# Kernel optimization log

Hardware: AMD Instinct MI355X
Metric: run time of the kernel (lower is better)

The kernel has to match this reference:

```python
import jax, jax.numpy as jnp
import numpy as np

NUM_HEADS, HEAD_SIZE = 8, 80
C = NUM_HEADS * HEAD_SIZE  # 640
GROUPS = 32
EPS = 1e-5


def group_norm(x, gamma, beta):
    b, h, w, c = x.shape
    xg = x.reshape(b, h, w, GROUPS, c // GROUPS)
    mean = xg.mean(axis=(1, 2, 4), keepdims=True)
    var = xg.var(axis=(1, 2, 4), keepdims=True)
    xg = (xg - mean) * jax.lax.rsqrt(var + EPS)
    return xg.reshape(b, h, w, c) * gamma + beta


def layer_norm(x, gamma, beta):
    mean = x.mean(axis=-1, keepdims=True)
    var = x.var(axis=-1, keepdims=True)
    return (x - mean) * jax.lax.rsqrt(var + EPS) * gamma + beta


def cross_attention(x, ctx, wq, wk, wv, wo, bo):
    # x: [B,S,C], ctx: [B,T,Cc]
    b, s, _ = x.shape
    t = ctx.shape[1]
    q = (x @ wq).reshape(b, s, NUM_HEADS, HEAD_SIZE)
    k = (ctx @ wk).reshape(b, t, NUM_HEADS, HEAD_SIZE)
    v = (ctx @ wv).reshape(b, t, NUM_HEADS, HEAD_SIZE)
    scale = HEAD_SIZE ** -0.5
    score = jnp.einsum('bqnh,bknh->bnqk', q, k) * scale
    weights = jax.nn.softmax(score, axis=-1)
    attn = jnp.einsum('bnqk,bknh->bqnh', weights, v)
    return attn.reshape(b, s, C) @ wo + bo


def geglu(x, w, b):
    p = x @ w + b
    xh, gate = p[..., :2560], p[..., 2560:]
    tanh_res = jnp.tanh(gate * 0.7978845608 * (1.0 + 0.044715 * gate * gate))
    return xh * 0.5 * gate * (1.0 + tanh_res)


def setup_inputs() -> dict:
    key = jax.random.key(0)
    ks = iter(jax.random.split(key, 32))
    rn = lambda shape, s=0.02: jax.random.normal(next(ks), shape, dtype=jnp.float32) * s
    inp = {
        'x': jax.random.normal(next(ks), (8, 32, 32, 640), dtype=jnp.float32),
        'context': jax.random.normal(next(ks), (8, 77, 768), dtype=jnp.float32),
        'gn_gamma': jnp.ones((640,), jnp.float32), 'gn_beta': jnp.zeros((640,), jnp.float32),
        'proj_in_w': rn((640, 640)), 'proj_in_b': jnp.zeros((640,), jnp.float32),
        'ln1_g': jnp.ones((640,), jnp.float32), 'ln1_b': jnp.zeros((640,), jnp.float32),
        'a1_q': rn((640, 640)), 'a1_k': rn((640, 640)), 'a1_v': rn((640, 640)),
        'a1_o': rn((640, 640)), 'a1_ob': jnp.zeros((640,), jnp.float32),
        'ln2_g': jnp.ones((640,), jnp.float32), 'ln2_b': jnp.zeros((640,), jnp.float32),
        'a2_q': rn((640, 640)), 'a2_k': rn((768, 640)), 'a2_v': rn((768, 640)),
        'a2_o': rn((640, 640)), 'a2_ob': jnp.zeros((640,), jnp.float32),
        'ln3_g': jnp.ones((640,), jnp.float32), 'ln3_b': jnp.zeros((640,), jnp.float32),
        'ff1_w': rn((640, 5120)), 'ff1_b': jnp.zeros((5120,), jnp.float32),
        'ff2_w': rn((2560, 640)), 'ff2_b': jnp.zeros((640,), jnp.float32),
        'proj_out_w': rn((640, 640)), 'proj_out_b': jnp.zeros((640,), jnp.float32),
    }
    return inp


def reference(x, context, gn_gamma, gn_beta, proj_in_w, proj_in_b,
              ln1_g, ln1_b, a1_q, a1_k, a1_v, a1_o, a1_ob,
              ln2_g, ln2_b, a2_q, a2_k, a2_v, a2_o, a2_ob,
              ln3_g, ln3_b, ff1_w, ff1_b, ff2_w, ff2_b,
              proj_out_w, proj_out_b):
    b, h, w, c = x.shape
    # GroupNorm + 1x1 conv proj_in (== dense over channels)
    y = group_norm(x, gn_gamma, gn_beta)
    y = y @ proj_in_w + proj_in_b
    y = y.reshape(b, h * w, c)
    # Transformer block
    t = cross_attention(layer_norm(y, ln1_g, ln1_b), layer_norm(y, ln1_g, ln1_b), a1_q, a1_k, a1_v, a1_o, a1_ob) + y
    t = cross_attention(layer_norm(t, ln2_g, ln2_b), context, a2_q, a2_k, a2_v, a2_o, a2_ob) + t
    t = geglu(layer_norm(t, ln3_g, ln3_b), ff1_w, ff1_b) @ ff2_w + ff2_b + t
    # proj_out (1x1 conv) + residual
    t = t.reshape(b, h, w, c)
    return t @ proj_out_w + proj_out_b + x
```

## Files before the change

kernel.cpp:

```cpp
#include <hip/hip_runtime.h>
#include <hip/hip_bf16.h>
#include <math.h>

typedef unsigned short u16;
typedef unsigned int u32;
typedef __attribute__((ext_vector_type(8))) short bf16x8;
typedef __attribute__((ext_vector_type(4))) float f32x4;

__device__ __forceinline__ u16 f2b(float f) {
    union { float f; unsigned u; } v; v.f = f;
    unsigned r = v.u + 0x7fffu + ((v.u >> 16) & 1u);
    return (u16)(r >> 16);
}
__device__ __forceinline__ float b2f(u16 h) {
    union { unsigned u; float f; } v; v.u = ((unsigned)h) << 16; return v.f;
}

__device__ __forceinline__ void gld16(const u16* gp, u16* lp) {
    auto g = (const __attribute__((address_space(1))) u32*)gp;
    auto l = (__attribute__((address_space(3))) u32*)lp;
    __builtin_amdgcn_global_load_lds(g, l, 16, 0, 0);
}

__device__ __forceinline__ int swz(int row, int q) { return (q + (row >> 1)) & 3; }

struct GemmP {
    const u16* A; const float* Af; const u16* B;
    const float* bias; const float* res;
    float* Cf; u16* Cb;
    int M, N, K, lda, ldb, ldc;
    float alpha;
};

__global__ __launch_bounds__(256) void gemm_bt(GemmP p) {
    __shared__ u16 As[128 * 32];
    __shared__ u16 Bs[128 * 32];
    const int tid = threadIdx.x;
    const int m0 = blockIdx.y * 128, n0 = blockIdx.x * 128;
    const int lane = tid & 63, wave = tid >> 6;
    const int quad = lane >> 4, l16 = lane & 15;
    const int wr = (wave >> 1) * 64, wc = (wave & 1) * 64;
    const int srow = lane >> 2, pcb = lane & 3;

    f32x4 acc[4][4];
#pragma unroll
    for (int i = 0; i < 4; i++)
#pragma unroll
        for (int j = 0; j < 4; j++) acc[i][j] = (f32x4){0.f, 0.f, 0.f, 0.f};

    for (int k0 = 0; k0 < p.K; k0 += 32) {
        if (p.Af) {
            int row = tid >> 1, half = tid & 1;
            const float* src = p.Af + (long)(m0 + row) * p.lda + k0 + half * 16;
            u16 tmp[16];
#pragma unroll
            for (int i2 = 0; i2 < 4; i2++) {
                float4 f = *(const float4*)(src + i2 * 4);
                tmp[i2 * 4 + 0] = f2b(f.x); tmp[i2 * 4 + 1] = f2b(f.y);
                tmp[i2 * 4 + 2] = f2b(f.z); tmp[i2 * 4 + 3] = f2b(f.w);
            }
            *(uint4*)&As[row * 32 + swz(row, 2 * half) * 8]     = *(uint4*)tmp;
            *(uint4*)&As[row * 32 + swz(row, 2 * half + 1) * 8] = *(uint4*)(tmp + 8);
#pragma unroll
            for (int j = 0; j < 2; j++) {
                int rbase = wave * 32 + j * 16;
                int r = rbase + srow;
                int lcb = (pcb - (r >> 1)) & 3;
                gld16(p.B + (long)(n0 + r) * p.ldb + k0 + lcb * 8, &Bs[rbase * 32]);
            }
        } else {
#pragma unroll
            for (int j = 0; j < 2; j++) {
                int rbase = wave * 32 + j * 16;
                int r = rbase + srow;
                int lcb = (pcb - (r >> 1)) & 3;
                gld16(p.A + (long)(m0 + r) * p.lda + k0 + lcb * 8, &As[rbase * 32]);
                gld16(p.B + (long)(n0 + r) * p.ldb + k0 + lcb * 8, &Bs[rbase * 32]);
            }
        }
        __syncthreads();

        bf16x8 af[4], bfr[4];
#pragma unroll
        for (int mi = 0; mi < 4; mi++) {
            int row = wr + mi * 16 + l16;
            af[mi] = *(const bf16x8*)&As[row * 32 + swz(row, quad) * 8];
        }
#pragma unroll
        for (int ni = 0; ni < 4; ni++) {
            int row = wc + ni * 16 + l16;
            bfr[ni] = *(const bf16x8*)&Bs[row * 32 + swz(row, quad) * 8];
        }
#pragma unroll
        for (int mi = 0; mi < 4; mi++)
#pragma unroll
            for (int ni = 0; ni < 4; ni++)
                acc[mi][ni] = __builtin_amdgcn_mfma_f32_16x16x32_bf16(af[mi], bfr[ni], acc[mi][ni], 0, 0, 0);
        __syncthreads();
    }

#pragma unroll
    for (int mi = 0; mi < 4; mi++) {
#pragma unroll
        for (int ni = 0; ni < 4; ni++) {
#pragma unroll
            for (int r = 0; r < 4; r++) {
                int row = m0 + wr + mi * 16 + quad * 4 + r;
                int col = n0 + wc + ni * 16 + l16;
                if (row < p.M && col < p.N) {
                    float v = acc[mi][ni][r] * p.alpha;
                    if (p.bias) v += p.bias[col];
                    long idx = (long)row * p.ldc + col;
                    if (p.res) v += p.res[idx];
                    if (p.Cf) p.Cf[idx] = v; else p.Cb[idx] = f2b(v);
                }
            }
        }
    }
}

struct GegluP {
    const u16* A; const u16* Bx; const u16* Bg;
    const float* bx; const float* bg;
    u16* H;
    int K, lda, ldb, ldh;
};

__global__ __launch_bounds__(256) void gemm_geglu(GegluP p) {
    __shared__ u16 As[128 * 32];
    __shared__ u16 Bxs[128 * 32];
    __shared__ u16 Bgs[128 * 32];
    const int tid = threadIdx.x;
    const int m0 = blockIdx.y * 128, n0 = blockIdx.x * 128;
    const int lane = tid & 63, wave = tid >> 6;
    const int quad = lane >> 4, l16 = lane & 15;
    const int wr = (wave >> 1) * 64, wc = (wave & 1) * 64;
    const int srow = lane >> 2, pcb = lane & 3;

    f32x4 ax[4][4], ag[4][4];
#pragma unroll
    for (int i = 0; i < 4; i++)
#pragma unroll
        for (int j = 0; j < 4; j++) { ax[i][j] = (f32x4){0.f,0.f,0.f,0.f}; ag[i][j] = (f32x4){0.f,0.f,0.f,0.f}; }

    for (int k0 = 0; k0 < p.K; k0 += 32) {
#pragma unroll
        for (int j = 0; j < 2; j++) {
            int rbase = wave * 32 + j * 16;
            int r = rbase + srow;
            int lcb = (pcb - (r >> 1)) & 3;
            gld16(p.A  + (long)(m0 + r) * p.lda + k0 + lcb * 8, &As[rbase * 32]);
            gld16(p.Bx + (long)(n0 + r) * p.ldb + k0 + lcb * 8, &Bxs[rbase * 32]);
            gld16(p.Bg + (long)(n0 + r) * p.ldb + k0 + lcb * 8, &Bgs[rbase * 32]);
        }
        __syncthreads();

        bf16x8 af[4], bxf[4], bgf[4];
#pragma unroll
        for (int mi = 0; mi < 4; mi++) {
            int row = wr + mi * 16 + l16;
            af[mi] = *(const bf16x8*)&As[row * 32 + swz(row, quad) * 8];
        }
#pragma unroll
        for (int ni = 0; ni < 4; ni++) {
            int row = wc + ni * 16 + l16;
            bxf[ni] = *(const bf16x8*)&Bxs[row * 32 + swz(row, quad) * 8];
            bgf[ni] = *(const bf16x8*)&Bgs[row * 32 + swz(row, quad) * 8];
        }
#pragma unroll
        for (int mi = 0; mi < 4; mi++)
#pragma unroll
            for (int ni = 0; ni < 4; ni++) {
                ax[mi][ni] = __builtin_amdgcn_mfma_f32_16x16x32_bf16(af[mi], bxf[ni], ax[mi][ni], 0, 0, 0);
                ag[mi][ni] = __builtin_amdgcn_mfma_f32_16x16x32_bf16(af[mi], bgf[ni], ag[mi][ni], 0, 0, 0);
            }
        __syncthreads();
    }

#pragma unroll
    for (int mi = 0; mi < 4; mi++) {
#pragma unroll
        for (int ni = 0; ni < 4; ni++) {
#pragma unroll
            for (int r = 0; r < 4; r++) {
                int row = m0 + wr + mi * 16 + quad * 4 + r;
                int col = wc + ni * 16 + l16;
                float xh = ax[mi][ni][r] + p.bx[n0 + col];
                float g  = ag[mi][ni][r] + p.bg[n0 + col];
                float u  = 0.7978845608f * g * (1.0f + 0.044715f * g * g);
                float s  = 1.0f / (1.0f + __expf(-2.0f * u));
                p.H[(long)row * p.ldh + n0 + col] = f2b(xh * g * s);
            }
        }
    }
}

struct FlashP {
    const u16* Q; const u16* K; const u16* V;
    u16* O;
    int ldq, ldk, ldv, ldo;
    int S, TS, nIter;
    long qBatch, kBatch;
    float scale;
};

__global__ __launch_bounds__(256, 2) void flash_attn(FlashP p) {
    __shared__ u16 shU[128 * 136];
    __shared__ u16 shV[80 * 136];
    const int z = blockIdx.z, b = z >> 3, h = z & 7;
    const int q0 = blockIdx.x * 128;
    const int tid = threadIdx.x, lane = tid & 63, w = tid >> 6;
    const int quad = lane >> 4, l16 = lane & 15;

    const u16* Qp = p.Q + (long)b * p.qBatch + (long)q0 * p.ldq + h * 80;
    const u16* Kp = p.K + (long)b * p.kBatch + h * 80;
    const u16* Vp = p.V + (long)b * p.kBatch + h * 80;

    for (int idx = tid; idx < 128 * 12; idx += 256) {
        int row = idx / 12, g = idx - row * 12;
        uint4 v = {0, 0, 0, 0};
        if (g < 10) v = *(const uint4*)(Qp + (long)row * p.ldq + g * 8);
        *(uint4*)&shU[row * 104 + g * 8] = v;
    }
    __syncthreads();
    bf16x8 qf[2][3];
#pragma unroll
    for (int mi = 0; mi < 2; mi++)
#pragma unroll
        for (int kk = 0; kk < 3; kk++)
            qf[mi][kk] = *(const bf16x8*)&shU[(w * 32 + mi * 16 + l16) * 104 + kk * 32 + quad * 8];
    __syncthreads();

    float m_[2][4], l_[2][4];
    f32x4 acc_o[2][5];
#pragma unroll
    for (int mi = 0; mi < 2; mi++) {
#pragma unroll
        for (int r = 0; r < 4; r++) { m_[mi][r] = -1e30f; l_[mi][r] = 0.f; }
#pragma unroll
        for (int ni = 0; ni < 5; ni++) acc_o[mi][ni] = (f32x4){0.f, 0.f, 0.f, 0.f};
    }

    for (int it = 0; it < p.nIter; it++) {
        const int s0 = it * 128;
        for (int idx = tid; idx < 128 * 12; idx += 256) {
            int row = idx / 12, g = idx - row * 12;
            uint4 v = {0, 0, 0, 0};
            if (g < 10 && (s0 + row) < p.TS)
                v = *(const uint4*)(Kp + (long)(s0 + row) * p.ldk + g * 8);
            *(uint4*)&shU[row * 104 + g * 8] = v;
        }
        for (int idx = tid; idx < 128 * 10; idx += 256) {
            int row = idx / 10, g = idx - row * 10;
            uint4 v = {0, 0, 0, 0};
            if ((s0 + row) < p.TS)
                v = *(const uint4*)(Vp + (long)(s0 + row) * p.ldv + g * 8);
            u16 tmp[8]; *(uint4*)tmp = v;
#pragma unroll
            for (int j = 0; j < 8; j++) shV[(g * 8 + j) * 136 + row] = tmp[j];
        }
        __syncthreads();

        f32x4 acc_s[2][8];
#pragma unroll
        for (int mi = 0; mi < 2; mi++)
#pragma unroll
            for (int ni = 0; ni < 8; ni++) acc_s[mi][ni] = (f32x4){0.f, 0.f, 0.f, 0.f};
#pragma unroll
        for (int kk = 0; kk < 3; kk++) {
            bf16x8 kf[8];
#pragma unroll
            for (int ni = 0; ni < 8; ni++)
                kf[ni] = *(const bf16x8*)&shU[(ni * 16 + l16) * 104 + kk * 32 + quad * 8];
#pragma unroll
            for (int mi = 0; mi < 2; mi++)
#pragma unroll
                for (int ni = 0; ni < 8; ni++)
                    acc_s[mi][ni] = __builtin_amdgcn_mfma_f32_16x16x32_bf16(qf[mi][kk], kf[ni], acc_s[mi][ni], 0, 0, 0);
        }
        __syncthreads();

#pragma unroll
        for (int mi = 0; mi < 2; mi++) {
#pragma unroll
            for (int ni = 0; ni < 8; ni++) {
                bool valid = (s0 + ni * 16 + l16) < p.TS;
#pragma unroll
                for (int r = 0; r < 4; r++)
                    acc_s[mi][ni][r] = valid ? acc_s[mi][ni][r] * p.scale : -1e30f;
            }
#pragma unroll
            for (int r = 0; r < 4; r++) {
                float rm = acc_s[mi][0][r];
#pragma unroll
                for (int ni = 1; ni < 8; ni++) rm = fmaxf(rm, acc_s[mi][ni][r]);
#pragma unroll
                for (int msk = 1; msk < 16; msk <<= 1) rm = fmaxf(rm, __shfl_xor(rm, msk));
                float mn = fmaxf(m_[mi][r], rm);
                float al = __expf(m_[mi][r] - mn);
                m_[mi][r] = mn;
                float rs = 0.f;
                int prow = (w * 32 + mi * 16 + quad * 4 + r) * 136;
#pragma unroll
                for (int ni = 0; ni < 8; ni++) {
                    float pv = __expf(acc_s[mi][ni][r] - mn);
                    rs += pv;
                    shU[prow + ni * 16 + l16] = f2b(pv);
                }
#pragma unroll
                for (int msk = 1; msk < 16; msk <<= 1) rs += __shfl_xor(rs, msk);
                l_[mi][r] = l_[mi][r] * al + rs;
#pragma unroll
                for (int ni = 0; ni < 5; ni++) acc_o[mi][ni][r] *= al;
            }
        }
        __syncthreads();

#pragma unroll
        for (int kk = 0; kk < 4; kk++) {
            bf16x8 vf[5], pf[2];
#pragma unroll
            for (int ni = 0; ni < 5; ni++)
                vf[ni] = *(const bf16x8*)&shV[(ni * 16 + l16) * 136 + kk * 32 + quad * 8];
#pragma unroll
            for (int mi = 0; mi < 2; mi++)
                pf[mi] = *(const bf16x8*)&shU[(w * 32 + mi * 16 + l16) * 136 + kk * 32 + quad * 8];
#pragma unroll
            for (int mi = 0; mi < 2; mi++)
#pragma unroll
                for (int ni = 0; ni < 5; ni++)
                    acc_o[mi][ni] = __builtin_amdgcn_mfma_f32_16x16x32_bf16(pf[mi], vf[ni], acc_o[mi][ni], 0, 0, 0);
        }
        __syncthreads();
    }

    u16* Op = p.O + ((long)b * p.S + q0) * p.ldo + h * 80;
#pragma unroll
    for (int mi = 0; mi < 2; mi++) {
#pragma unroll
        for (int r = 0; r < 4; r++) {
            float inv = 1.0f / l_[mi][r];
            int row = w * 32 + mi * 16 + quad * 4 + r;
#pragma unroll
            for (int ni = 0; ni < 5; ni++)
                Op[(long)row * p.ldo + ni * 16 + l16] = f2b(acc_o[mi][ni][r] * inv);
        }
    }
}

struct WT8 { const float* W[8]; u16* Wt[8]; };

__global__ void wtrans8(WT8 p, int K, int N) {
    __shared__ float tile[32][33];
    const float* W = p.W[blockIdx.z];
    u16* Wt = p.Wt[blockIdx.z];
    int n0 = blockIdx.x * 32, k0 = blockIdx.y * 32;
    int tx = threadIdx.x, ty = threadIdx.y;
#pragma unroll
    for (int i = 0; i < 4; i++) {
        int k = k0 + ty + i * 8, n = n0 + tx;
        if (k < K && n < N) tile[ty + i * 8][tx] = W[(long)k * N + n];
    }
    __syncthreads();
#pragma unroll
    for (int i = 0; i < 4; i++) {
        int n = n0 + ty + i * 8, k = k0 + tx;
        if (n < N && k < K) Wt[(long)n * K + k] = f2b(tile[tx][ty + i * 8]);
    }
}

__global__ void gn_stats(const float* __restrict__ x, float* __restrict__ stats) {
    int bid = blockIdx.x;
    int b = bid >> 5, g = bid & 31;
    const float* base = x + (long)b * 32 * 32 * 640 + g * 20;
    float s = 0.f, sq = 0.f;
    for (int idx = threadIdx.x; idx < 32 * 32 * 20; idx += 256) {
        int hw = idx / 20, c = idx - hw * 20;
        float v = base[(long)hw * 640 + c];
        s += v; sq += v * v;
    }
    __shared__ float rs[256], rq[256];
    rs[threadIdx.x] = s; rq[threadIdx.x] = sq; __syncthreads();
    for (int t = 128; t > 0; t >>= 1) {
        if (threadIdx.x < t) { rs[threadIdx.x] += rs[threadIdx.x + t]; rq[threadIdx.x] += rq[threadIdx.x + t]; }
        __syncthreads();
    }
    if (threadIdx.x == 0) {
        float mean = rs[0] / 20480.0f;
        float var = rq[0] / 20480.0f - mean * mean;
        stats[bid * 2] = mean;
        stats[bid * 2 + 1] = rsqrtf(var + 1e-5f);
    }
}

__global__ void gn_apply(const float* __restrict__ x, const float* __restrict__ stats,
                         const float* __restrict__ gamma, const float* __restrict__ beta,
                         u16* __restrict__ out) {
    long i = (long)blockIdx.x * 256 + threadIdx.x;
    int c = (int)(i % 640);
    int b = (int)(i / (32 * 32 * 640));
    int g = c / 20;
    float mean = stats[(b * 32 + g) * 2], inv = stats[(b * 32 + g) * 2 + 1];
    out[i] = f2b((x[i] - mean) * inv * gamma[c] + beta[c]);
}

__global__ void layernorm_rows(const float* __restrict__ X, const float* __restrict__ g,
                               const float* __restrict__ be, u16* __restrict__ out, int nrows) {
    int row = blockIdx.x * 4 + (threadIdx.x >> 6);
    int lane = threadIdx.x & 63;
    if (row >= nrows) return;
    const float* x = X + (long)row * 640;
    float v[10];
    float s = 0.f;
#pragma unroll
    for (int i = 0; i < 10; i++) { v[i] = x[lane + i * 64]; s += v[i]; }
#pragma unroll
    for (int m = 1; m < 64; m <<= 1) s += __shfl_xor(s, m);
    float mean = s * (1.0f / 640.0f);
    float sq = 0.f;
#pragma unroll
    for (int i = 0; i < 10; i++) { float d = v[i] - mean; sq += d * d; }
#pragma unroll
    for (int m = 1; m < 64; m <<= 1) sq += __shfl_xor(sq, m);
    float inv = rsqrtf(sq * (1.0f / 640.0f) + 1e-5f);
    u16* o = out + (long)row * 640;
#pragma unroll
    for (int i = 0; i < 10; i++) {
        int c = lane + i * 64;
        o[c] = f2b((v[i] - mean) * inv * g[c] + be[c]);
    }
}

__global__ void f2b_k(const float* __restrict__ src, u16* __restrict__ dst, long n) {
    long i = (long)blockIdx.x * 256 + threadIdx.x;
    if (i < n) dst[i] = f2b(src[i]);
}

extern "C" void kernel_launch(void* const* d_in, const int* in_sizes, int n_in,
                              void* d_out, int out_size, void* d_ws, size_t ws_size,
                              hipStream_t stream) {
    const float* x        = (const float*)d_in[0];
    const float* context  = (const float*)d_in[1];
    const float* gn_gamma = (const float*)d_in[2];
    const float* gn_beta  = (const float*)d_in[3];
    const float* proj_in_w = (const float*)d_in[4];
    const float* proj_in_b = (const float*)d_in[5];
    const float* ln1_g = (const float*)d_in[6];
    const float* ln1_b = (const float*)d_in[7];
    const float* a1_q = (const float*)d_in[8];
    const float* a1_k = (const float*)d_in[9];
    const float* a1_v = (const float*)d_in[10];
    const float* a1_o = (const float*)d_in[11];
    const float* a1_ob = (const float*)d_in[12];
    const float* ln2_g = (const float*)d_in[13];
    const float* ln2_b = (const float*)d_in[14];
    const float* a2_q = (const float*)d_in[15];
    const float* a2_k = (const float*)d_in[16];
    const float* a2_v = (const float*)d_in[17];
    const float* a2_o = (const float*)d_in[18];
    const float* a2_ob = (const float*)d_in[19];
    const float* ln3_g = (const float*)d_in[20];
    const float* ln3_b = (const float*)d_in[21];
    const float* ff1_w = (const float*)d_in[22];
    const float* ff1_b = (const float*)d_in[23];
    const float* ff2_w = (const float*)d_in[24];
    const float* ff2_b = (const float*)d_in[25];
    const float* proj_out_w = (const float*)d_in[26];
    const float* proj_out_b = (const float*)d_in[27];
    float* out = (float*)d_out;

    char* ws = (char*)d_ws;
    size_t off = 0;
    auto alloc = [&](size_t bytes) -> void* {
        void* p = ws + off;
        off += (bytes + 255) & ~(size_t)255;
        return p;
    };
    u16* Wt_pi  = (u16*)alloc(640 * 640 * 2);
    u16* Wt_qkv = (u16*)alloc((size_t)1920 * 640 * 2);
    u16* Wt_1o  = (u16*)alloc(640 * 640 * 2);
    u16* Wt_2q  = (u16*)alloc(640 * 640 * 2);
    u16* Wt_kv2 = (u16*)alloc((size_t)1280 * 768 * 2);
    u16* Wt_2o  = (u16*)alloc(640 * 640 * 2);
    u16* Wt_f1  = (u16*)alloc((size_t)5120 * 640 * 2);
    u16* Wt_f2  = (u16*)alloc((size_t)640 * 2560 * 2);
    u16* Wt_po  = (u16*)alloc(640 * 640 * 2);
    float* t    = (float*)alloc((size_t)8192 * 640 * 4);
    u16* bufA   = (u16*)alloc((size_t)8192 * 640 * 2);
    u16* big    = (u16*)alloc((size_t)8192 * 2560 * 2);
    u16* kv2b   = (u16*)alloc((size_t)616 * 1280 * 2);
    u16* ctxb   = (u16*)alloc((size_t)616 * 768 * 2);
    float* stats = (float*)alloc(256 * 2 * 4);
    (void)alloc(65536);
    u16* qkvb = big;
    u16* hb   = big;

    const float SCALE = 0.11180339887498949f;

    auto gemm1 = [&](const u16* A, const float* Af, const u16* Bt, const float* bias,
                     const float* res, float* Cf, u16* Cb, int M, int N, int K,
                     int lda, int ldb, int ldc, float alpha) {
        GemmP p{};
        p.A = A; p.Af = Af; p.B = Bt; p.bias = bias; p.res = res; p.Cf = Cf; p.Cb = Cb;
        p.M = M; p.N = N; p.K = K; p.lda = lda; p.ldb = ldb; p.ldc = ldc;
        p.alpha = alpha;
        dim3 grid((N + 127) / 128, (M + 127) / 128, 1);
        gemm_bt<<<grid, 256, 0, stream>>>(p);
    };

    {
        dim3 blk(32, 8);
        WT8 sq{};
        sq.W[0] = proj_in_w; sq.Wt[0] = Wt_pi;
        sq.W[1] = a1_q;      sq.Wt[1] = Wt_qkv;
        sq.W[2] = a1_k;      sq.Wt[2] = Wt_qkv + 640 * 640;
        sq.W[3] = a1_v;      sq.Wt[3] = Wt_qkv + 2 * 640 * 640;
        sq.W[4] = a1_o;      sq.Wt[4] = Wt_1o;
        sq.W[5] = a2_q;      sq.Wt[5] = Wt_2q;
        sq.W[6] = a2_o;      sq.Wt[6] = Wt_2o;
        sq.W[7] = proj_out_w; sq.Wt[7] = Wt_po;
        wtrans8<<<dim3(20, 20, 8), blk, 0, stream>>>(sq, 640, 640);
        WT8 kv{};
        kv.W[0] = a2_k; kv.Wt[0] = Wt_kv2;
        kv.W[1] = a2_v; kv.Wt[1] = Wt_kv2 + (size_t)640 * 768;
        wtrans8<<<dim3(20, 24, 2), blk, 0, stream>>>(kv, 768, 640);
        WT8 f1{}; f1.W[0] = ff1_w; f1.Wt[0] = Wt_f1;
        wtrans8<<<dim3(160, 20, 1), blk, 0, stream>>>(f1, 640, 5120);
        WT8 f2{}; f2.W[0] = ff2_w; f2.Wt[0] = Wt_f2;
        wtrans8<<<dim3(20, 80, 1), blk, 0, stream>>>(f2, 2560, 640);
    }

    gn_stats<<<256, 256, 0, stream>>>(x, stats);
    gn_apply<<<20480, 256, 0, stream>>>(x, stats, gn_gamma, gn_beta, bufA);
    gemm1(bufA, nullptr, Wt_pi, proj_in_b, nullptr, t, nullptr, 8192, 640, 640, 640, 640, 640, 1.0f);

    layernorm_rows<<<2048, 256, 0, stream>>>(t, ln1_g, ln1_b, bufA, 8192);
    gemm1(bufA, nullptr, Wt_qkv, nullptr, nullptr, nullptr, qkvb, 8192, 1920, 640, 640, 640, 1920, 1.0f);
    {
        FlashP p{};
        p.Q = qkvb; p.K = qkvb + 640; p.V = qkvb + 1280; p.O = bufA;
        p.ldq = 1920; p.ldk = 1920; p.ldv = 1920; p.ldo = 640;
        p.S = 1024; p.TS = 1024; p.nIter = 8;
        p.qBatch = (long)1024 * 1920; p.kBatch = (long)1024 * 1920;
        p.scale = SCALE;
        flash_attn<<<dim3(8, 1, 64), 256, 0, stream>>>(p);
    }
    gemm1(bufA, nullptr, Wt_1o, a1_ob, t, t, nullptr, 8192, 640, 640, 640, 640, 640, 1.0f);

    layernorm_rows<<<2048, 256, 0, stream>>>(t, ln2_g, ln2_b, bufA, 8192);
    f2b_k<<<1848, 256, 0, stream>>>(context, ctxb, 473088);
    gemm1(bufA, nullptr, Wt_2q, nullptr, nullptr, nullptr, qkvb, 8192, 640, 640, 640, 640, 640, 1.0f);
    gemm1(ctxb, nullptr, Wt_kv2, nullptr, nullptr, nullptr, kv2b, 616, 1280, 768, 768, 768, 1280, 1.0f);
    {
        FlashP p{};
        p.Q = qkvb; p.K = kv2b; p.V = kv2b + 640; p.O = bufA;
        p.ldq = 640; p.ldk = 1280; p.ldv = 1280; p.ldo = 640;
        p.S = 1024; p.TS = 77; p.nIter = 1;
        p.qBatch = (long)1024 * 640; p.kBatch = (long)77 * 1280;
        p.scale = SCALE;
        flash_attn<<<dim3(8, 1, 64), 256, 0, stream>>>(p);
    }
    gemm1(bufA, nullptr, Wt_2o, a2_ob, t, t, nullptr, 8192, 640, 640, 640, 640, 640, 1.0f);

    layernorm_rows<<<2048, 256, 0, stream>>>(t, ln3_g, ln3_b, bufA, 8192);
    {
        GegluP p{};
        p.A = bufA; p.Bx = Wt_f1; p.Bg = Wt_f1 + (size_t)2560 * 640;
        p.bx = ff1_b; p.bg = ff1_b + 2560;
        p.H = hb;
        p.K = 640; p.lda = 640; p.ldb = 640; p.ldh = 2560;
        gemm_geglu<<<dim3(20, 64), 256, 0, stream>>>(p);
    }
    gemm1(hb, nullptr, Wt_f2, ff2_b, t, t, nullptr, 8192, 640, 2560, 2560, 2560, 640, 1.0f);

    gemm1(nullptr, t, Wt_po, proj_out_b, x, out, nullptr, 8192, 640, 640, 640, 640, 640, 1.0f);
}
```

Before: 852.0 us.

## Double GEMM K-tile to 64, add 64-row M tile, reorder flash grid

The GEMM and GEGLU kernels now stage a 64-wide K slice per iteration with an 8-way swizzle, halving the number of barrier pairs per K loop. gemm_bt is templated on M tile size, and the N=640 GEMMs use 64-row tiles to launch more blocks and fill more CUs. The flash attention grid swaps its x and z dimensions so consecutive blocks cover different batch-heads. In exchange, LDS use per block roughly doubles, which may lower occupancy, and the smaller tiles reduce operand reuse.

```diff
diff --git a/kernel.cpp b/kernel.cpp
--- a/kernel.cpp
+++ b/kernel.cpp
@@ -22,7 +22,7 @@
     __builtin_amdgcn_global_load_lds(g, l, 16, 0, 0);
 }
 
-__device__ __forceinline__ int swz(int row, int q) { return (q + (row >> 1)) & 3; }
+__device__ __forceinline__ int swz8(int row, int lb) { return (lb + (row >> 1)) & 7; }
 
 struct GemmP {
     const u16* A; const float* Af; const u16* B;
@@ -32,75 +32,82 @@
     float alpha;
 };
 
+template<int MT>
 __global__ __launch_bounds__(256) void gemm_bt(GemmP p) {
-    __shared__ u16 As[128 * 32];
-    __shared__ u16 Bs[128 * 32];
+    constexpr int MI = MT / 32;
+    __shared__ u16 As[MT * 64];
+    __shared__ u16 Bs[128 * 64];
     const int tid = threadIdx.x;
-    const int m0 = blockIdx.y * 128, n0 = blockIdx.x * 128;
+    const int m0 = blockIdx.y * MT, n0 = blockIdx.x * 128;
     const int lane = tid & 63, wave = tid >> 6;
     const int quad = lane >> 4, l16 = lane & 15;
-    const int wr = (wave >> 1) * 64, wc = (wave & 1) * 64;
-    const int srow = lane >> 2, pcb = lane & 3;
-
-    f32x4 acc[4][4];
-#pragma unroll
-    for (int i = 0; i < 4; i++)
+    const int wr = (wave >> 1) * (MT / 2), wc = (wave & 1) * 64;
+    const int srow = lane >> 3, pb8 = lane & 7;
+
+    f32x4 acc[MI][4];
+#pragma unroll
+    for (int i = 0; i < MI; i++)
 #pragma unroll
         for (int j = 0; j < 4; j++) acc[i][j] = (f32x4){0.f, 0.f, 0.f, 0.f};
 
-    for (int k0 = 0; k0 < p.K; k0 += 32) {
+    for (int k0 = 0; k0 < p.K; k0 += 64) {
         if (p.Af) {
-            int row = tid >> 1, half = tid & 1;
-            const float* src = p.Af + (long)(m0 + row) * p.lda + k0 + half * 16;
-            u16 tmp[16];
-#pragma unroll
-            for (int i2 = 0; i2 < 4; i2++) {
-                float4 f = *(const float4*)(src + i2 * 4);
-                tmp[i2 * 4 + 0] = f2b(f.x); tmp[i2 * 4 + 1] = f2b(f.y);
-                tmp[i2 * 4 + 2] = f2b(f.z); tmp[i2 * 4 + 3] = f2b(f.w);
-            }
-            *(uint4*)&As[row * 32 + swz(row, 2 * half) * 8]     = *(uint4*)tmp;
-            *(uint4*)&As[row * 32 + swz(row, 2 * half + 1) * 8] = *(uint4*)(tmp + 8);
-#pragma unroll
-            for (int j = 0; j < 2; j++) {
-                int rbase = wave * 32 + j * 16;
+            constexpr int TPR = 256 / MT;
+            constexpr int NB = 8 / TPR;
+            int row = tid / TPR, part = tid % TPR;
+            const float* srcr = p.Af + (long)(m0 + row) * p.lda + k0;
+#pragma unroll
+            for (int q2 = 0; q2 < NB; q2++) {
+                int lb = part * NB + q2;
+                float4 f0 = *(const float4*)(srcr + lb * 8);
+                float4 f1 = *(const float4*)(srcr + lb * 8 + 4);
+                u16 tmp[8];
+                tmp[0]=f2b(f0.x); tmp[1]=f2b(f0.y); tmp[2]=f2b(f0.z); tmp[3]=f2b(f0.w);
+                tmp[4]=f2b(f1.x); tmp[5]=f2b(f1.y); tmp[6]=f2b(f1.z); tmp[7]=f2b(f1.w);
+                *(uint4*)&As[row * 64 + swz8(row, lb) * 8] = *(uint4*)tmp;
+            }
+        } else {
+#pragma unroll
+            for (int j = 0; j < MT / 32; j++) {
+                int rbase = wave * (MT / 4) + j * 8;
                 int r = rbase + srow;
-                int lcb = (pcb - (r >> 1)) & 3;
-                gld16(p.B + (long)(n0 + r) * p.ldb + k0 + lcb * 8, &Bs[rbase * 32]);
-            }
-        } else {
-#pragma unroll
-            for (int j = 0; j < 2; j++) {
-                int rbase = wave * 32 + j * 16;
-                int r = rbase + srow;
-                int lcb = (pcb - (r >> 1)) & 3;
-                gld16(p.A + (long)(m0 + r) * p.lda + k0 + lcb * 8, &As[rbase * 32]);
-                gld16(p.B + (long)(n0 + r) * p.ldb + k0 + lcb * 8, &Bs[rbase * 32]);
-            }
-        }
-        __syncthreads();
-
-        bf16x8 af[4], bfr[4];
-#pragma unroll
-        for (int mi = 0; mi < 4; mi++) {
-            int row = wr + mi * 16 + l16;
-            af[mi] = *(const bf16x8*)&As[row * 32 + swz(row, quad) * 8];
-        }
-#pragma unroll
-        for (int ni = 0; ni < 4; ni++) {
-            int row = wc + ni * 16 + l16;
-            bfr[ni] = *(const bf16x8*)&Bs[row * 32 + swz(row, quad) * 8];
-        }
-#pragma unroll
-        for (int mi = 0; mi < 4; mi++)
-#pragma unroll
-            for (int ni = 0; ni < 4; ni++)
-                acc[mi][ni] = __builtin_amdgcn_mfma_f32_16x16x32_bf16(af[mi], bfr[ni], acc[mi][ni], 0, 0, 0);
-        __syncthreads();
-    }
-
-#pragma unroll
-    for (int mi = 0; mi < 4; mi++) {
+                int lb = (pb8 - (r >> 1)) & 7;
+                gld16(p.A + (long)(m0 + r) * p.lda + k0 + lb * 8, &As[rbase * 64]);
+            }
+        }
+#pragma unroll
+        for (int j = 0; j < 4; j++) {
+            int rbase = wave * 32 + j * 8;
+            int r = rbase + srow;
+            int lb = (pb8 - (r >> 1)) & 7;
+            gld16(p.B + (long)(n0 + r) * p.ldb + k0 + lb * 8, &Bs[rbase * 64]);
+        }
+        __syncthreads();
+
+#pragma unroll
+        for (int kk = 0; kk < 2; kk++) {
+            bf16x8 af[MI], bfr[4];
+#pragma unroll
+            for (int mi = 0; mi < MI; mi++) {
+                int row = wr + mi * 16 + l16;
+                af[mi] = *(const bf16x8*)&As[row * 64 + swz8(row, kk * 4 + quad) * 8];
+            }
+#pragma unroll
+            for (int ni = 0; ni < 4; ni++) {
+                int row = wc + ni * 16 + l16;
+                bfr[ni] = *(const bf16x8*)&Bs[row * 64 + swz8(row, kk * 4 + quad) * 8];
+            }
+#pragma unroll
+            for (int mi = 0; mi < MI; mi++)
+#pragma unroll
+                for (int ni = 0; ni < 4; ni++)
+                    acc[mi][ni] = __builtin_amdgcn_mfma_f32_16x16x32_bf16(af[mi], bfr[ni], acc[mi][ni], 0, 0, 0);
+        }
+        __syncthreads();
+    }
+
+#pragma unroll
+    for (int mi = 0; mi < MI; mi++) {
 #pragma unroll
         for (int ni = 0; ni < 4; ni++) {
 #pragma unroll
@@ -127,15 +134,15 @@
 };
 
 __global__ __launch_bounds__(256) void gemm_geglu(GegluP p) {
-    __shared__ u16 As[128 * 32];
-    __shared__ u16 Bxs[128 * 32];
-    __shared__ u16 Bgs[128 * 32];
+    __shared__ u16 As[128 * 64];
+    __shared__ u16 Bxs[128 * 64];
+    __shared__ u16 Bgs[128 * 64];
     const int tid = threadIdx.x;
     const int m0 = blockIdx.y * 128, n0 = blockIdx.x * 128;
     const int lane = tid & 63, wave = tid >> 6;
     const int quad = lane >> 4, l16 = lane & 15;
     const int wr = (wave >> 1) * 64, wc = (wave & 1) * 64;
-    const int srow = lane >> 2, pcb = lane & 3;
+    const int srow = lane >> 3, pb8 = lane & 7;
 
     f32x4 ax[4][4], ag[4][4];
 #pragma unroll
@@ -143,37 +150,40 @@
 #pragma unroll
         for (int j = 0; j < 4; j++) { ax[i][j] = (f32x4){0.f,0.f,0.f,0.f}; ag[i][j] = (f32x4){0.f,0.f,0.f,0.f}; }
 
-    for (int k0 = 0; k0 < p.K; k0 += 32) {
-#pragma unroll
-        for (int j = 0; j < 2; j++) {
-            int rbase = wave * 32 + j * 16;
+    for (int k0 = 0; k0 < p.K; k0 += 64) {
+#pragma unroll
+        for (int j = 0; j < 4; j++) {
+            int rbase = wave * 32 + j * 8;
             int r = rbase + srow;
-            int lcb = (pcb - (r >> 1)) & 3;
-            gld16(p.A  + (long)(m0 + r) * p.lda + k0 + lcb * 8, &As[rbase * 32]);
-            gld16(p.Bx + (long)(n0 + r) * p.ldb + k0 + lcb * 8, &Bxs[rbase * 32]);
-            gld16(p.Bg + (long)(n0 + r) * p.ldb + k0 + lcb * 8, &Bgs[rbase * 32]);
-        }
-        __syncthreads();
-
-        bf16x8 af[4], bxf[4], bgf[4];
-#pragma unroll
-        for (int mi = 0; mi < 4; mi++) {
-            int row = wr + mi * 16 + l16;
-            af[mi] = *(const bf16x8*)&As[row * 32 + swz(row, quad) * 8];
-        }
-#pragma unroll
-        for (int ni = 0; ni < 4; ni++) {
-            int row = wc + ni * 16 + l16;
-            bxf[ni] = *(const bf16x8*)&Bxs[row * 32 + swz(row, quad) * 8];
-            bgf[ni] = *(const bf16x8*)&Bgs[row * 32 + swz(row, quad) * 8];
-        }
-#pragma unroll
-        for (int mi = 0; mi < 4; mi++)
+            int lb = (pb8 - (r >> 1)) & 7;
+            gld16(p.A  + (long)(m0 + r) * p.lda + k0 + lb * 8, &As[rbase * 64]);
+            gld16(p.Bx + (long)(n0 + r) * p.ldb + k0 + lb * 8, &Bxs[rbase * 64]);
+            gld16(p.Bg + (long)(n0 + r) * p.ldb + k0 + lb * 8, &Bgs[rbase * 64]);
+        }
+        __syncthreads();
+
+#pragma unroll
+        for (int kk = 0; kk < 2; kk++) {
+            bf16x8 af[4], bxf[4], bgf[4];
+#pragma unroll
+            for (int mi = 0; mi < 4; mi++) {
+                int row = wr + mi * 16 + l16;
+                af[mi] = *(const bf16x8*)&As[row * 64 + swz8(row, kk * 4 + quad) * 8];
+            }
 #pragma unroll
             for (int ni = 0; ni < 4; ni++) {
-                ax[mi][ni] = __builtin_amdgcn_mfma_f32_16x16x32_bf16(af[mi], bxf[ni], ax[mi][ni], 0, 0, 0);
-                ag[mi][ni] = __builtin_amdgcn_mfma_f32_16x16x32_bf16(af[mi], bgf[ni], ag[mi][ni], 0, 0, 0);
-            }
+                int row = wc + ni * 16 + l16;
+                bxf[ni] = *(const bf16x8*)&Bxs[row * 64 + swz8(row, kk * 4 + quad) * 8];
+                bgf[ni] = *(const bf16x8*)&Bgs[row * 64 + swz8(row, kk * 4 + quad) * 8];
+            }
+#pragma unroll
+            for (int mi = 0; mi < 4; mi++)
+#pragma unroll
+                for (int ni = 0; ni < 4; ni++) {
+                    ax[mi][ni] = __builtin_amdgcn_mfma_f32_16x16x32_bf16(af[mi], bxf[ni], ax[mi][ni], 0, 0, 0);
+                    ag[mi][ni] = __builtin_amdgcn_mfma_f32_16x16x32_bf16(af[mi], bgf[ni], ag[mi][ni], 0, 0, 0);
+                }
+        }
         __syncthreads();
     }
 
@@ -207,8 +217,8 @@
 __global__ __launch_bounds__(256, 2) void flash_attn(FlashP p) {
     __shared__ u16 shU[128 * 136];
     __shared__ u16 shV[80 * 136];
-    const int z = blockIdx.z, b = z >> 3, h = z & 7;
-    const int q0 = blockIdx.x * 128;
+    const int z = blockIdx.x, b = z >> 3, h = z & 7;
+    const int q0 = blockIdx.z * 128;
     const int tid = threadIdx.x, lane = tid & 63, w = tid >> 6;
     const int quad = lane >> 4, l16 = lane & 15;
 
@@ -499,13 +509,14 @@
 
     auto gemm1 = [&](const u16* A, const float* Af, const u16* Bt, const float* bias,
                      const float* res, float* Cf, u16* Cb, int M, int N, int K,
-                     int lda, int ldb, int ldc, float alpha) {
+                     int lda, int ldb, int ldc, float alpha, int mt) {
         GemmP p{};
         p.A = A; p.Af = Af; p.B = Bt; p.bias = bias; p.res = res; p.Cf = Cf; p.Cb = Cb;
         p.M = M; p.N = N; p.K = K; p.lda = lda; p.ldb = ldb; p.ldc = ldc;
         p.alpha = alpha;
-        dim3 grid((N + 127) / 128, (M + 127) / 128, 1);
-        gemm_bt<<<grid, 256, 0, stream>>>(p);
+        dim3 grid((N + 127) / 128, (M + mt - 1) / mt, 1);
+        if (mt == 64) gemm_bt<64><<<grid, 256, 0, stream>>>(p);
+        else          gemm_bt<128><<<grid, 256, 0, stream>>>(p);
     };
 
     {
@@ -532,10 +543,10 @@
 
     gn_stats<<<256, 256, 0, stream>>>(x, stats);
     gn_apply<<<20480, 256, 0, stream>>>(x, stats, gn_gamma, gn_beta, bufA);
-    gemm1(bufA, nullptr, Wt_pi, proj_in_b, nullptr, t, nullptr, 8192, 640, 640, 640, 640, 640, 1.0f);
+    gemm1(bufA, nullptr, Wt_pi, proj_in_b, nullptr, t, nullptr, 8192, 640, 640, 640, 640, 640, 1.0f, 64);
 
     layernorm_rows<<<2048, 256, 0, stream>>>(t, ln1_g, ln1_b, bufA, 8192);
-    gemm1(bufA, nullptr, Wt_qkv, nullptr, nullptr, nullptr, qkvb, 8192, 1920, 640, 640, 640, 1920, 1.0f);
+    gemm1(bufA, nullptr, Wt_qkv, nullptr, nullptr, nullptr, qkvb, 8192, 1920, 640, 640, 640, 1920, 1.0f, 128);
     {
         FlashP p{};
         p.Q = qkvb; p.K = qkvb + 640; p.V = qkvb + 1280; p.O = bufA;
@@ -543,14 +554,14 @@
         p.S = 1024; p.TS = 1024; p.nIter = 8;
         p.qBatch = (long)1024 * 1920; p.kBatch = (long)1024 * 1920;
         p.scale = SCALE;
-        flash_attn<<<dim3(8, 1, 64), 256, 0, stream>>>(p);
-    }
-    gemm1(bufA, nullptr, Wt_1o, a1_ob, t, t, nullptr, 8192, 640, 640, 640, 640, 640, 1.0f);
+        flash_attn<<<dim3(64, 1, 8), 256, 0, stream>>>(p);
+    }
+    gemm1(bufA, nullptr, Wt_1o, a1_ob, t, t, nullptr, 8192, 640, 640, 640, 640, 640, 1.0f, 64);
 
     layernorm_rows<<<2048, 256, 0, stream>>>(t, ln2_g, ln2_b, bufA, 8192);
     f2b_k<<<1848, 256, 0, stream>>>(context, ctxb, 473088);
-    gemm1(bufA, nullptr, Wt_2q, nullptr, nullptr, nullptr, qkvb, 8192, 640, 640, 640, 640, 640, 1.0f);
-    gemm1(ctxb, nullptr, Wt_kv2, nullptr, nullptr, nullptr, kv2b, 616, 1280, 768, 768, 768, 1280, 1.0f);
+    gemm1(bufA, nullptr, Wt_2q, nullptr, nullptr, nullptr, qkvb, 8192, 640, 640, 640, 640, 640, 1.0f, 64);
+    gemm1(ctxb, nullptr, Wt_kv2, nullptr, nullptr, nullptr, kv2b, 616, 1280, 768, 768, 768, 1280, 1.0f, 64);
     {
         FlashP p{};
         p.Q = qkvb; p.K = kv2b; p.V = kv2b + 640; p.O = bufA;
@@ -558,9 +569,9 @@
         p.S = 1024; p.TS = 77; p.nIter = 1;
         p.qBatch = (long)1024 * 640; p.kBatch = (long)77 * 1280;
         p.scale = SCALE;
-        flash_attn<<<dim3(8, 1, 64), 256, 0, stream>>>(p);
-    }
-    gemm1(bufA, nullptr, Wt_2o, a2_ob, t, t, nullptr, 8192, 640, 640, 640, 640, 640, 1.0f);
+        flash_attn<<<dim3(64, 1, 8), 256, 0, stream>>>(p);
+    }
+    gemm1(bufA, nullptr, Wt_2o, a2_ob, t, t, nullptr, 8192, 640, 640, 640, 640, 640, 1.0f, 64);
 
     layernorm_rows<<<2048, 256, 0, stream>>>(t, ln3_g, ln3_b, bufA, 8192);
     {
@@ -571,7 +582,7 @@
         p.K = 640; p.lda = 640; p.ldb = 640; p.ldh = 2560;
         gemm_geglu<<<dim3(20, 64), 256, 0, stream>>>(p);
     }
-    gemm1(hb, nullptr, Wt_f2, ff2_b, t, t, nullptr, 8192, 640, 2560, 2560, 2560, 640, 1.0f);
-
-    gemm1(nullptr, t, Wt_po, proj_out_b, x, out, nullptr, 8192, 640, 640, 640, 640, 640, 1.0f);
-}
+    gemm1(hb, nullptr, Wt_f2, ff2_b, t, t, nullptr, 8192, 640, 2560, 2560, 2560, 640, 1.0f, 64);
+
+    gemm1(nullptr, t, Wt_po, proj_out_b, x, out, nullptr, 8192, 640, 640, 640, 640, 640, 1.0f, 64);
+}
```

Result: faster. 699.7 us (-17.9%).
